# Kernel optimization log

Hardware: AMD Instinct MI355X
Metric: run time of the kernel (lower is better)

The kernel has to match this reference:

```python
import jax, jax.numpy as jnp
import numpy as np

NC, ND, B, K = 10000, 1000000, 8192, 64
EMB = 16
CH_DENSE, DEV_DENSE = 16, 20
CAT_MAX = [100, 4, 50, 200, 500, 1000, 300]  # lang, plat, os, country, carrier, brand, plat_os
H1, H2, ATTN_H = 64, 64, 84
IN1 = CH_DENSE + EMB        # 32  (channel dense + channel_id emb)
IN2 = DEV_DENSE + 7 * EMB   # 132 (device dense + 7 cat embs)


def setup_inputs() -> dict:
    key = jax.random.key(0)
    ks = jax.random.split(key, 32)
    def nrm(k, shape, s=0.05):
        return jax.random.normal(k, shape, dtype=jnp.float32) * s
    inp = {}
    inp["channel_dense"] = nrm(ks[0], (NC, CH_DENSE), 1.0)
    inp["device_dense"] = nrm(ks[1], (ND, DEV_DENSE), 1.0)
    inp["channel_id_emb"] = nrm(ks[2], (NC, EMB))
    names = ["lang_emb", "plat_emb", "os_emb", "country_emb", "carrier_emb", "brand_emb", "plat_os_emb"]
    for i, (n, m) in enumerate(zip(names, CAT_MAX)):
        inp[n] = nrm(ks[3 + i], (m, EMB))
    inp["W_agg"] = nrm(ks[10], (IN2, H2));  inp["b_agg"] = jnp.zeros((H2,), jnp.float32)
    inp["W_self"] = nrm(ks[11], (IN1, H1)); inp["b_self"] = jnp.zeros((H1,), jnp.float32)
    inp["W_attn"] = nrm(ks[12], (H2 + IN1, ATTN_H)); inp["b_attn"] = jnp.zeros((ATTN_H,), jnp.float32)
    inp["W_attn2"] = nrm(ks[13], (ATTN_H, 1)); inp["b_attn2"] = jnp.zeros((1,), jnp.float32)
    inp["channel_ids"] = jax.random.randint(ks[14], (NC,), 0, NC)
    cat_cols = [jax.random.randint(ks[15 + i], (ND,), 0, m) for i, m in enumerate(CAT_MAX)]
    inp["device_cat"] = jnp.stack(cat_cols, axis=1)  # [ND, 7]
    inp["vertices"] = jax.random.randint(ks[22], (B,), 0, NC)
    inp["bot_neibrs"] = jax.random.randint(ks[23], (B, K), 0, ND)
    inp["normal_neibrs"] = jax.random.randint(ks[24], (B, K), 0, ND)
    inp["bot_counts"] = jax.random.randint(ks[25], (B,), 1, K + 1)
    inp["normal_counts"] = jax.random.randint(ks[26], (B,), 1, K + 1)
    return inp


def reference(channel_dense, device_dense, channel_id_emb, lang_emb, plat_emb, os_emb,
              country_emb, carrier_emb, brand_emb, plat_os_emb,
              W_agg, b_agg, W_self, b_self, W_attn, b_attn, W_attn2, b_attn2,
              channel_ids, device_cat, vertices, bot_neibrs, normal_neibrs,
              bot_counts, normal_counts):
    cat_tables = [lang_emb, plat_emb, os_emb, country_emb, carrier_emb, brand_emb, plat_os_emb]
    # channel self features: dense cols + channel_id embedding  -> [B, IN1]
    ch_v = jnp.concatenate([channel_dense[vertices],
                            channel_id_emb[channel_ids[vertices]]], axis=1)

    def agg(neibrs, counts):
        # gather neighbor device features, embed categoricals, masked mean, linear (Mean_agg)
        dense = device_dense[neibrs]                                   # [B, K, DEV_DENSE]
        cats = device_cat[neibrs]                                      # [B, K, 7]
        embs = jnp.concatenate([t[cats[..., i]] for i, t in enumerate(cat_tables)], axis=-1)
        feats = jnp.concatenate([dense, embs], axis=-1)                # [B, K, IN2]
        mask = (jnp.arange(K)[None, :] < counts[:, None]).astype(feats.dtype)
        mean = jnp.sum(feats * mask[..., None], axis=1) / jnp.maximum(counts, 1).astype(feats.dtype)[:, None]
        return mean @ W_agg + b_agg                                    # [B, H2]

    bots = agg(bot_neibrs, bot_counts)
    normal = agg(normal_neibrs, normal_counts)

    def score(h):
        # attention MLP on concat(aggregated feats, channel self feats)
        return jax.nn.relu(jnp.concatenate([h, ch_v], axis=1) @ W_attn + b_attn) @ W_attn2 + b_attn2

    a = jax.nn.softmax(jnp.concatenate([score(bots), score(normal)], axis=1), axis=1)  # [B, 2]
    gcn = a[:, 0:1] * bots + a[:, 1:2] * normal                        # convex combination [B, H2]
    # Msg_out: relu(concat(agg_out, linear(self)))
    return jax.nn.relu(jnp.concatenate([gcn, ch_v @ W_self + b_self], axis=1))  # [B, H2+H1]
```

## Files before the change

### kernel.cpp

```cpp
#include <hip/hip_runtime.h>

#define BATCH 8192
#define KNB   64
#define EMB   16
#define CHD   16
#define DVD   20
#define H1    64
#define H2    64
#define AH    84
#define IN1   32
#define IN2   132

#define RB 32
#define VB 16

__global__ __launch_bounds__(256) void gconv_gather(
    const float* __restrict__ device_dense,
    const float* __restrict__ t0, const float* __restrict__ t1,
    const float* __restrict__ t2, const float* __restrict__ t3,
    const float* __restrict__ t4, const float* __restrict__ t5,
    const float* __restrict__ t6,
    const int* __restrict__ device_cat,
    const int* __restrict__ bot_neibrs,
    const int* __restrict__ normal_neibrs,
    const int* __restrict__ bot_counts,
    const int* __restrict__ normal_counts,
    float* __restrict__ fsum_ws)
{
    const int b    = blockIdx.x;
    const int v    = b >> 1;
    const int half = b & 1;
    const int t    = threadIdx.x;
    const int w    = t >> 6;
    const int L    = t & 63;

    __shared__ alignas(16) int   ofs[KNB][8];
    __shared__ alignas(16) float psum[4][IN2];

    const int* neibrs = half ? normal_neibrs : bot_neibrs;
    int cnt = half ? normal_counts[v] : bot_counts[v];
    if (cnt > KNB) cnt = KNB;
    if (cnt < 1)   cnt = 1;

    if (t < KNB) {
        int n = 0;
        if (t < cnt) n = neibrs[v * KNB + t];
        const long cb = (long)n * 7;
        const int c0 = device_cat[cb + 0];
        const int c1 = device_cat[cb + 1];
        const int c2 = device_cat[cb + 2];
        const int c3 = device_cat[cb + 3];
        const int c4 = device_cat[cb + 4];
        const int c5 = device_cat[cb + 5];
        const int c6 = device_cat[cb + 6];
        *(int4*)&ofs[t][0] = make_int4(n * DVD, c0 * EMB, c1 * EMB, c2 * EMB);
        *(int4*)&ofs[t][4] = make_int4(c3 * EMB, c4 * EMB, c5 * EMB, c6 * EMB);
    }
    __syncthreads();

    const int kk   = L >> 5;
    const int slot = L & 31;
    const float* P; int sIdx, c4v;
    if (slot < 5) {
        P = device_dense; sIdx = 0; c4v = slot * 4;
    } else {
        const int e = slot - 5;
        const int tsel = e >> 2;
        c4v = (e & 3) * 4; sIdx = 1 + tsel;
        switch (tsel) {
            case 0: P = t0; break;
            case 1: P = t1; break;
            case 2: P = t2; break;
            case 3: P = t3; break;
            case 4: P = t4; break;
            case 5: P = t5; break;
            default: P = t6; break;
        }
    }
    const bool xa = (slot == 0);

    float4 acc  = make_float4(0.f, 0.f, 0.f, 0.f);
    float4 accx = make_float4(0.f, 0.f, 0.f, 0.f);

    for (int i0 = 0; i0 < 8; i0 += 4) {
        if (2 * w + 8 * i0 >= cnt) break;
        int o[4], ox[4];
        #pragma unroll
        for (int i = 0; i < 4; ++i) {
            const int k = 2 * w + 8 * (i0 + i) + kk;
            o[i]  = ofs[k][sIdx];
            ox[i] = ofs[k][7];
        }
        __builtin_amdgcn_sched_barrier(0);
        float4 val[4], vx[4];
        #pragma unroll
        for (int i = 0; i < 4; ++i)
            val[i] = *(const float4*)(P + o[i] + c4v);
        if (xa) {
            #pragma unroll
            for (int i = 0; i < 4; ++i)
                vx[i] = *(const float4*)(t6 + ox[i] + 12);
        }
        __builtin_amdgcn_sched_barrier(0);
        #pragma unroll
        for (int i = 0; i < 4; ++i) {
            const int k = 2 * w + 8 * (i0 + i) + kk;
            const float m = (k < cnt) ? 1.f : 0.f;
            acc.x = fmaf(m, val[i].x, acc.x);
            acc.y = fmaf(m, val[i].y, acc.y);
            acc.z = fmaf(m, val[i].z, acc.z);
            acc.w = fmaf(m, val[i].w, acc.w);
            if (xa) {
                accx.x = fmaf(m, vx[i].x, accx.x);
                accx.y = fmaf(m, vx[i].y, accx.y);
                accx.z = fmaf(m, vx[i].z, accx.z);
                accx.w = fmaf(m, vx[i].w, accx.w);
            }
        }
    }

    acc.x += __shfl_xor(acc.x, 32, 64);
    acc.y += __shfl_xor(acc.y, 32, 64);
    acc.z += __shfl_xor(acc.z, 32, 64);
    acc.w += __shfl_xor(acc.w, 32, 64);
    accx.x += __shfl_xor(accx.x, 32, 64);
    accx.y += __shfl_xor(accx.y, 32, 64);
    accx.z += __shfl_xor(accx.z, 32, 64);
    accx.w += __shfl_xor(accx.w, 32, 64);

    if (L < 32) *(float4*)&psum[w][slot * 4] = acc;
    if (L == 0) *(float4*)&psum[w][128]      = accx;
    __syncthreads();

    if (t < IN2)
        fsum_ws[(size_t)b * IN2 + t] =
            psum[0][t] + psum[1][t] + psum[2][t] + psum[3][t];
}

__global__ __launch_bounds__(256) void gconv_dense(
    const float* __restrict__ channel_dense,
    const float* __restrict__ channel_id_emb,
    const float* __restrict__ W_agg,  const float* __restrict__ b_agg,
    const float* __restrict__ W_self, const float* __restrict__ b_self,
    const float* __restrict__ W_attn, const float* __restrict__ b_attn,
    const float* __restrict__ W_attn2,
    const int* __restrict__ channel_ids,
    const int* __restrict__ vertices,
    const int* __restrict__ bot_counts,
    const int* __restrict__ normal_counts,
    const float* __restrict__ fsum_ws,
    float* __restrict__ out)
{
    const int blk = blockIdx.x;
    const int b0  = blk * RB;
    const int v0  = blk * VB;
    const int t   = threadIdx.x;

    __shared__ alignas(16) float fs[RB][IN2];
    __shared__ alignas(16) float chvs[VB][IN1];
    __shared__ alignas(16) float hs[RB][H2];
    __shared__ float u_lds[AH][RB + 1];
    __shared__ float sarr[RB];
    __shared__ float cinv[RB];

    for (int idx = t; idx < RB * IN2 / 4; idx += 256) {
        const float4 vv = *(const float4*)(fsum_ws + (size_t)b0 * IN2 + idx * 4);
        *(float4*)&((float*)fs)[idx * 4] = vv;
    }
    if (t < RB) {
        const int b = b0 + t;
        const int v = b >> 1;
        int c = (b & 1) ? normal_counts[v] : bot_counts[v];
        c = (c > KNB) ? KNB : ((c < 1) ? 1 : c);
        cinv[t] = 1.0f / (float)c;
    }
    if (t < 128) {
        const int vx = t >> 3, q = t & 7;
        const int vert = vertices[v0 + vx];
        const float* src = (q < 4)
            ? channel_dense  + (size_t)vert * CHD + q * 4
            : channel_id_emb + (size_t)channel_ids[vert] * EMB + (q - 4) * 4;
        *(float4*)&chvs[vx][q * 4] = *(const float4*)src;
    }
    __syncthreads();

    {
        const int w = t >> 6, lane = t & 63;
        const int r0 = w * 8;
        float acc[8] = {0.f, 0.f, 0.f, 0.f, 0.f, 0.f, 0.f, 0.f};
        #pragma unroll 4
        for (int f = 0; f < IN2; ++f) {
            const float wv = W_agg[f * H2 + lane];
            #pragma unroll
            for (int r = 0; r < 8; ++r)
                acc[r] = fmaf(fs[r0 + r][f], wv, acc[r]);
        }
        const float bb = b_agg[lane];
        #pragma unroll
        for (int r = 0; r < 8; ++r)
            hs[r0 + r][lane] = fmaf(acc[r], cinv[r0 + r], bb);
    }
    __syncthreads();

    if (t < 2 * AH) {
        const int rg = (t >= AH) ? 1 : 0;
        const int aa = t - AH * rg;
        const int r0 = rg * 16;
        float acc[16];
        #pragma unroll
        for (int r = 0; r < 16; ++r) acc[r] = 0.f;
        #pragma unroll 2
        for (int f = 0; f < H2; ++f) {
            const float wv = W_attn[f * AH + aa];
            #pragma unroll
            for (int r = 0; r < 16; ++r)
                acc[r] = fmaf(hs[r0 + r][f], wv, acc[r]);
        }
        #pragma unroll 2
        for (int f = 0; f < IN1; ++f) {
            const float wv = W_attn[(H2 + f) * AH + aa];
            #pragma unroll
            for (int r = 0; r < 16; ++r)
                acc[r] = fmaf(chvs[(r0 + r) >> 1][f], wv, acc[r]);
        }
        const float ba = b_attn[aa], w2 = W_attn2[aa];
        #pragma unroll
        for (int r = 0; r < 16; ++r)
            u_lds[aa][r0 + r] = fmaxf(acc[r] + ba, 0.f) * w2;
    }
    __syncthreads();

    if (t < RB) {
        float s = 0.f;
        #pragma unroll 4
        for (int aa = 0; aa < AH; ++aa) s += u_lds[aa][t];
        sarr[t] = s;
    }
    __syncthreads();

    {
        const int vl = t >> 4;
        const int c8 = (t & 15) * 8;
        const float s0 = sarr[2 * vl], s1 = sarr[2 * vl + 1];
        const float mm = fmaxf(s0, s1);
        const float e0 = __expf(s0 - mm), e1 = __expf(s1 - mm);
        const float rs = 1.0f / (e0 + e1);
        const float a0 = e0 * rs, a1 = e1 * rs;
        float o[8];
        if (c8 < H2) {
            #pragma unroll
            for (int c = 0; c < 8; ++c)
                o[c] = fmaxf(a0 * hs[2 * vl][c8 + c] + a1 * hs[2 * vl + 1][c8 + c], 0.f);
        } else {
            const int cs = c8 - H2;
            float accS[8];
            #pragma unroll
            for (int c = 0; c < 8; ++c) accS[c] = b_self[cs + c];
            #pragma unroll 4
            for (int f = 0; f < IN1; ++f) {
                const float xv = chvs[vl][f];
                const float4 wa = *(const float4*)(W_self + f * H1 + cs);
                const float4 wb = *(const float4*)(W_self + f * H1 + cs + 4);
                accS[0] = fmaf(xv, wa.x, accS[0]);
                accS[1] = fmaf(xv, wa.y, accS[1]);
                accS[2] = fmaf(xv, wa.z, accS[2]);
                accS[3] = fmaf(xv, wa.w, accS[3]);
                accS[4] = fmaf(xv, wb.x, accS[4]);
                accS[5] = fmaf(xv, wb.y, accS[5]);
                accS[6] = fmaf(xv, wb.z, accS[6]);
                accS[7] = fmaf(xv, wb.w, accS[7]);
            }
            #pragma unroll
            for (int c = 0; c < 8; ++c) o[c] = fmaxf(accS[c], 0.f);
        }
        float4* op = (float4*)(out + (size_t)(v0 + vl) * (H1 + H2) + c8);
        op[0] = make_float4(o[0], o[1], o[2], o[3]);
        op[1] = make_float4(o[4], o[5], o[6], o[7]);
    }
}

extern "C" void kernel_launch(void* const* d_in, const int* in_sizes, int n_in,
                              void* d_out, int out_size, void* d_ws, size_t ws_size,
                              hipStream_t stream) {
    const float* channel_dense  = (const float*)d_in[0];
    const float* device_dense   = (const float*)d_in[1];
    const float* channel_id_emb = (const float*)d_in[2];
    const float* lang_emb       = (const float*)d_in[3];
    const float* plat_emb       = (const float*)d_in[4];
    const float* os_emb         = (const float*)d_in[5];
    const float* country_emb    = (const float*)d_in[6];
    const float* carrier_emb    = (const float*)d_in[7];
    const float* brand_emb      = (const float*)d_in[8];
    const float* plat_os_emb    = (const float*)d_in[9];
    const float* W_agg          = (const float*)d_in[10];
    const float* b_agg          = (const float*)d_in[11];
    const float* W_self         = (const float*)d_in[12];
    const float* b_self         = (const float*)d_in[13];
    const float* W_attn         = (const float*)d_in[14];
    const float* b_attn         = (const float*)d_in[15];
    const float* W_attn2        = (const float*)d_in[16];
    const int* channel_ids   = (const int*)d_in[18];
    const int* device_cat    = (const int*)d_in[19];
    const int* vertices      = (const int*)d_in[20];
    const int* bot_neibrs    = (const int*)d_in[21];
    const int* normal_neibrs = (const int*)d_in[22];
    const int* bot_counts    = (const int*)d_in[23];
    const int* normal_counts = (const int*)d_in[24];

    float* fsum_ws = (float*)d_ws;
    float* out     = (float*)d_out;

    gconv_gather<<<dim3(2 * BATCH), dim3(256), 0, stream>>>(
        device_dense, lang_emb, plat_emb, os_emb, country_emb, carrier_emb,
        brand_emb, plat_os_emb, device_cat, bot_neibrs, normal_neibrs,
        bot_counts, normal_counts, fsum_ws);

    gconv_dense<<<dim3(2 * BATCH / RB), dim3(256), 0, stream>>>(
        channel_dense, channel_id_emb, W_agg, b_agg, W_self, b_self,
        W_attn, b_attn, W_attn2, channel_ids, vertices,
        bot_counts, normal_counts, fsum_ws, out);
}
```

Before: 76.81 us.

## Process multiple rows per gather block with double-buffered index staging and LDS plat table

Each gather block now handles eight (vertex, half) rows instead of one. It prefetches the next row's neighbor and category offsets into a second shared buffer while accumulating the current row. The tiny 4-row platform embedding table is cached in LDS, and its lookups are served by otherwise-idle lanes, which removes the extra lane-0 global load. Category indices are loaded as two overlapping int4 vectors. This cuts launch and block-setup overhead and hides index-fetch latency, at the cost of extra barriers per row and fewer total blocks for latency hiding.

```diff
diff --git a/kernel.cpp b/kernel.cpp
--- a/kernel.cpp
+++ b/kernel.cpp
@@ -13,6 +13,8 @@
 
 #define RB 32
 #define VB 16
+#define NIT 8
+#define NBLK (2 * BATCH / NIT)
 
 __global__ __launch_bounds__(256) void gconv_gather(
     const float* __restrict__ device_dense,
@@ -27,114 +29,144 @@
     const int* __restrict__ normal_counts,
     float* __restrict__ fsum_ws)
 {
-    const int b    = blockIdx.x;
-    const int v    = b >> 1;
-    const int half = b & 1;
+    const int blk  = blockIdx.x;
     const int t    = threadIdx.x;
     const int w    = t >> 6;
     const int L    = t & 63;
-
-    __shared__ alignas(16) int   ofs[KNB][8];
-    __shared__ alignas(16) float psum[4][IN2];
-
-    const int* neibrs = half ? normal_neibrs : bot_neibrs;
-    int cnt = half ? normal_counts[v] : bot_counts[v];
-    if (cnt > KNB) cnt = KNB;
-    if (cnt < 1)   cnt = 1;
-
-    if (t < KNB) {
-        int n = 0;
-        if (t < cnt) n = neibrs[v * KNB + t];
-        const long cb = (long)n * 7;
-        const int c0 = device_cat[cb + 0];
-        const int c1 = device_cat[cb + 1];
-        const int c2 = device_cat[cb + 2];
-        const int c3 = device_cat[cb + 3];
-        const int c4 = device_cat[cb + 4];
-        const int c5 = device_cat[cb + 5];
-        const int c6 = device_cat[cb + 6];
-        *(int4*)&ofs[t][0] = make_int4(n * DVD, c0 * EMB, c1 * EMB, c2 * EMB);
-        *(int4*)&ofs[t][4] = make_int4(c3 * EMB, c4 * EMB, c5 * EMB, c6 * EMB);
-    }
-    __syncthreads();
-
     const int kk   = L >> 5;
     const int slot = L & 31;
-    const float* P; int sIdx, c4v;
-    if (slot < 5) {
-        P = device_dense; sIdx = 0; c4v = slot * 4;
-    } else {
-        const int e = slot - 5;
-        const int tsel = e >> 2;
-        c4v = (e & 3) * 4; sIdx = 1 + tsel;
-        switch (tsel) {
+
+    __shared__ alignas(16) int   ofs[2][KNB][8];
+    __shared__ alignas(16) float psum[4][IN2];
+    __shared__ alignas(16) float plat_lds[64];
+    __shared__ int scnt[2];
+
+    if (t < 64) plat_lds[t] = t1[t];
+
+    const float* P = device_dense;
+    int sIdx = 0, c4v = slot * 4, fb = slot * 4;
+    if (slot >= 5 && slot < 29) {
+        const int e  = slot - 5;
+        const int tb = e >> 2;
+        c4v  = (e & 3) * 4;
+        sIdx = (tb == 0) ? 1 : (tb + 2);
+        fb   = 20 + 16 * ((tb == 0) ? 0 : tb + 1) + c4v;
+        switch (tb) {
             case 0: P = t0; break;
-            case 1: P = t1; break;
-            case 2: P = t2; break;
-            case 3: P = t3; break;
-            case 4: P = t4; break;
-            case 5: P = t5; break;
+            case 1: P = t2; break;
+            case 2: P = t3; break;
+            case 3: P = t4; break;
+            case 4: P = t5; break;
             default: P = t6; break;
         }
     }
-    const bool xa = (slot == 0);
-
-    float4 acc  = make_float4(0.f, 0.f, 0.f, 0.f);
-    float4 accx = make_float4(0.f, 0.f, 0.f, 0.f);
-
-    for (int i0 = 0; i0 < 8; i0 += 4) {
-        if (2 * w + 8 * i0 >= cnt) break;
-        int o[4], ox[4];
+    const bool isPlat = (slot >= 29);
+    const int  pcol   = (slot - 29) * 4;
+    if (isPlat) fb = 36 + pcol;
+
+    auto stage = [&](int it, int buf) {
+        if (w != (it & 3)) return;
+        const int b  = blk * NIT + it;
+        const int v  = b >> 1;
+        const bool nh = b & 1;
+        int cnt = nh ? normal_counts[v] : bot_counts[v];
+        cnt = cnt < 1 ? 1 : (cnt > KNB ? KNB : cnt);
+        int n = 0;
+        if (L < cnt) n = (nh ? normal_neibrs : bot_neibrs)[v * KNB + L];
+        const long cb = (long)n * 7;
+        const int4 cA = *(const int4*)(device_cat + cb);
+        const int4 cB = *(const int4*)(device_cat + cb + 3);
+        *(int4*)&ofs[buf][L][0] = make_int4(n * DVD, cA.x * EMB, cA.y * EMB, cA.z * EMB);
+        *(int4*)&ofs[buf][L][4] = make_int4(cA.w * EMB, cB.y * EMB, cB.z * EMB, cB.w * EMB);
+        if (L == 0) scnt[buf] = cnt;
+    };
+
+    stage(0, 0);
+    __syncthreads();
+
+    int buf = 0;
+    for (int it = 0; it < NIT; ++it) {
+        if (it + 1 < NIT) stage(it + 1, buf ^ 1);
+
+        const int cnt = scnt[buf];
+        float4 acc  = make_float4(0.f, 0.f, 0.f, 0.f);
+        float4 accx = make_float4(0.f, 0.f, 0.f, 0.f);
+
         #pragma unroll
-        for (int i = 0; i < 4; ++i) {
-            const int k = 2 * w + 8 * (i0 + i) + kk;
-            o[i]  = ofs[k][sIdx];
-            ox[i] = ofs[k][7];
-        }
-        __builtin_amdgcn_sched_barrier(0);
-        float4 val[4], vx[4];
-        #pragma unroll
-        for (int i = 0; i < 4; ++i)
-            val[i] = *(const float4*)(P + o[i] + c4v);
-        if (xa) {
-            #pragma unroll
-            for (int i = 0; i < 4; ++i)
-                vx[i] = *(const float4*)(t6 + ox[i] + 12);
-        }
-        __builtin_amdgcn_sched_barrier(0);
-        #pragma unroll
-        for (int i = 0; i < 4; ++i) {
-            const int k = 2 * w + 8 * (i0 + i) + kk;
-            const float m = (k < cnt) ? 1.f : 0.f;
-            acc.x = fmaf(m, val[i].x, acc.x);
-            acc.y = fmaf(m, val[i].y, acc.y);
-            acc.z = fmaf(m, val[i].z, acc.z);
-            acc.w = fmaf(m, val[i].w, acc.w);
-            if (xa) {
-                accx.x = fmaf(m, vx[i].x, accx.x);
-                accx.y = fmaf(m, vx[i].y, accx.y);
-                accx.z = fmaf(m, vx[i].z, accx.z);
-                accx.w = fmaf(m, vx[i].w, accx.w);
+        for (int c0 = 0; c0 < 8; c0 += 4) {
+            if (2 * w + 8 * c0 >= cnt) break;
+            const int kb = 2 * w + kk;
+            if (!isPlat) {
+                int o[4];
+                #pragma unroll
+                for (int i = 0; i < 4; ++i)
+                    o[i] = ofs[buf][kb + 8 * (c0 + i)][sIdx];
+                __builtin_amdgcn_sched_barrier(0);
+                float4 val[4];
+                #pragma unroll
+                for (int i = 0; i < 4; ++i)
+                    val[i] = *(const float4*)(P + o[i] + c4v);
+                __builtin_amdgcn_sched_barrier(0);
+                #pragma unroll
+                for (int i = 0; i < 4; ++i) {
+                    const float m = (kb + 8 * (c0 + i) < cnt) ? 1.f : 0.f;
+                    acc.x = fmaf(m, val[i].x, acc.x);
+                    acc.y = fmaf(m, val[i].y, acc.y);
+                    acc.z = fmaf(m, val[i].z, acc.z);
+                    acc.w = fmaf(m, val[i].w, acc.w);
+                }
+            } else {
+                #pragma unroll
+                for (int i = 0; i < 4; ++i) {
+                    const int k = kb + 8 * (c0 + i);
+                    const int o = ofs[buf][k][2];
+                    const float m = (k < cnt) ? 1.f : 0.f;
+                    const float4 pv = *(const float4*)&plat_lds[o + pcol];
+                    acc.x = fmaf(m, pv.x, acc.x);
+                    acc.y = fmaf(m, pv.y, acc.y);
+                    acc.z = fmaf(m, pv.z, acc.z);
+                    acc.w = fmaf(m, pv.w, acc.w);
+                    if (slot == 29) {
+                        const float4 pw = *(const float4*)&plat_lds[o + 12];
+                        accx.x = fmaf(m, pw.x, accx.x);
+                        accx.y = fmaf(m, pw.y, accx.y);
+                        accx.z = fmaf(m, pw.z, accx.z);
+                        accx.w = fmaf(m, pw.w, accx.w);
+                    }
+                }
             }
         }
-    }
-
-    acc.x += __shfl_xor(acc.x, 32, 64);
-    acc.y += __shfl_xor(acc.y, 32, 64);
-    acc.z += __shfl_xor(acc.z, 32, 64);
-    acc.w += __shfl_xor(acc.w, 32, 64);
-    accx.x += __shfl_xor(accx.x, 32, 64);
-    accx.y += __shfl_xor(accx.y, 32, 64);
-    accx.z += __shfl_xor(accx.z, 32, 64);
-    accx.w += __shfl_xor(accx.w, 32, 64);
-
-    if (L < 32) *(float4*)&psum[w][slot * 4] = acc;
-    if (L == 0) *(float4*)&psum[w][128]      = accx;
-    __syncthreads();
-
-    if (t < IN2)
-        fsum_ws[(size_t)b * IN2 + t] =
-            psum[0][t] + psum[1][t] + psum[2][t] + psum[3][t];
+
+        acc.x += __shfl_xor(acc.x, 32, 64);
+        acc.y += __shfl_xor(acc.y, 32, 64);
+        acc.z += __shfl_xor(acc.z, 32, 64);
+        acc.w += __shfl_xor(acc.w, 32, 64);
+        accx.x += __shfl_xor(accx.x, 32, 64);
+        accx.y += __shfl_xor(accx.y, 32, 64);
+        accx.z += __shfl_xor(accx.z, 32, 64);
+        accx.w += __shfl_xor(accx.w, 32, 64);
+
+        if (L < 32) {
+            *(float4*)&psum[w][fb] = acc;
+            if (slot == 29) *(float4*)&psum[w][48] = accx;
+        }
+        __syncthreads();
+
+        if (t < IN2 / 4) {
+            const float4 p0 = *(const float4*)&psum[0][t * 4];
+            const float4 p1 = *(const float4*)&psum[1][t * 4];
+            const float4 p2 = *(const float4*)&psum[2][t * 4];
+            const float4 p3 = *(const float4*)&psum[3][t * 4];
+            const int b = blk * NIT + it;
+            *(float4*)(fsum_ws + (size_t)b * IN2 + t * 4) =
+                make_float4(p0.x + p1.x + p2.x + p3.x,
+                            p0.y + p1.y + p2.y + p3.y,
+                            p0.z + p1.z + p2.z + p3.z,
+                            p0.w + p1.w + p2.w + p3.w);
+        }
+        __syncthreads();
+        buf ^= 1;
+    }
 }
 
 __global__ __launch_bounds__(256) void gconv_dense(
@@ -310,7 +342,7 @@
     float* fsum_ws = (float*)d_ws;
     float* out     = (float*)d_out;
 
-    gconv_gather<<<dim3(2 * BATCH), dim3(256), 0, stream>>>(
+    gconv_gather<<<dim3(NBLK), dim3(256), 0, stream>>>(
         device_dense, lang_emb, plat_emb, os_emb, country_emb, carrier_emb,
         brand_emb, plat_os_emb, device_cat, bot_neibrs, normal_neibrs,
         bot_counts, normal_counts, fsum_ws);
```

Measured after the change: 75.98 us. About the same (-1.1%).

## Assign one wavefront per neighbor list in gather kernel, removing block syncs

Applied to the files above, without the earlier changes.

The gather kernel now gives each wavefront its own (vertex, half) item, so one block of four wavefronts handles four items instead of one. Each wave builds its own offset table in LDS and waits on lgkmcnt instead of a block barrier. It loops over all its neighbors with an 8-deep unrolled load batch and writes results straight to the workspace, with no cross-wave LDS reduction. The leftover 16-byte slot of the last table is now computed with a full wave shuffle reduction, and the category reads are vectorized int4 loads. The intent is to remove __syncthreads and block-level reduction overhead and to raise memory-level parallelism per wave. The cost is that each wave now does more serial work per item. The int4 load at offset cb+3 reads misaligned addresses, and LDS writes and reads are not fenced across lanes except through the waitcnt.

```diff
diff --git a/kernel.cpp b/kernel.cpp
--- a/kernel.cpp
+++ b/kernel.cpp
@@ -27,47 +27,42 @@
     const int* __restrict__ normal_counts,
     float* __restrict__ fsum_ws)
 {
-    const int b    = blockIdx.x;
-    const int v    = b >> 1;
-    const int half = b & 1;
     const int t    = threadIdx.x;
     const int w    = t >> 6;
     const int L    = t & 63;
-
-    __shared__ alignas(16) int   ofs[KNB][8];
-    __shared__ alignas(16) float psum[4][IN2];
-
-    const int* neibrs = half ? normal_neibrs : bot_neibrs;
-    int cnt = half ? normal_counts[v] : bot_counts[v];
-    if (cnt > KNB) cnt = KNB;
-    if (cnt < 1)   cnt = 1;
-
-    if (t < KNB) {
-        int n = 0;
-        if (t < cnt) n = neibrs[v * KNB + t];
-        const long cb = (long)n * 7;
-        const int c0 = device_cat[cb + 0];
-        const int c1 = device_cat[cb + 1];
-        const int c2 = device_cat[cb + 2];
-        const int c3 = device_cat[cb + 3];
-        const int c4 = device_cat[cb + 4];
-        const int c5 = device_cat[cb + 5];
-        const int c6 = device_cat[cb + 6];
-        *(int4*)&ofs[t][0] = make_int4(n * DVD, c0 * EMB, c1 * EMB, c2 * EMB);
-        *(int4*)&ofs[t][4] = make_int4(c3 * EMB, c4 * EMB, c5 * EMB, c6 * EMB);
-    }
-    __syncthreads();
-
     const int kk   = L >> 5;
     const int slot = L & 31;
-    const float* P; int sIdx, c4v;
+    const int item = blockIdx.x * 4 + w;
+    const int v    = item >> 1;
+
+    __shared__ alignas(16) int ofs[4][KNB][8];
+
+    int cnt = (item & 1) ? normal_counts[v] : bot_counts[v];
+    cnt = cnt < 1 ? 1 : (cnt > KNB ? KNB : cnt);
+    cnt = __builtin_amdgcn_readfirstlane(cnt);
+
+    {
+        const int* nb = (item & 1) ? normal_neibrs : bot_neibrs;
+        const int n = (L < cnt) ? nb[v * KNB + L] : 0;
+        const long cb = (long)n * 7;
+        const int4 cA = *(const int4*)(device_cat + cb);
+        const int4 cB = *(const int4*)(device_cat + cb + 3);
+        *(int4*)&ofs[w][L][0] = make_int4(n * DVD, cA.x * EMB, cA.y * EMB, cA.z * EMB);
+        *(int4*)&ofs[w][L][4] = make_int4(cA.w * EMB, cB.y * EMB, cB.z * EMB, cB.w * EMB);
+    }
+    __asm__ volatile("s_waitcnt lgkmcnt(0)" ::: "memory");
+    __builtin_amdgcn_sched_barrier(0);
+
+    const float* P;
+    int oIdx, col, feat;
     if (slot < 5) {
-        P = device_dense; sIdx = 0; c4v = slot * 4;
+        P = device_dense; oIdx = 0; col = slot * 4; feat = slot * 4;
     } else {
-        const int e = slot - 5;
-        const int tsel = e >> 2;
-        c4v = (e & 3) * 4; sIdx = 1 + tsel;
-        switch (tsel) {
+        const int e  = slot - 5;
+        const int tb = e >> 2;
+        const int q  = e & 3;
+        oIdx = 1 + tb; col = 4 * q; feat = 20 + 16 * tb + 4 * q;
+        switch (tb) {
             case 0: P = t0; break;
             case 1: P = t1; break;
             case 2: P = t2; break;
@@ -77,45 +72,27 @@
             default: P = t6; break;
         }
     }
-    const bool xa = (slot == 0);
-
-    float4 acc  = make_float4(0.f, 0.f, 0.f, 0.f);
-    float4 accx = make_float4(0.f, 0.f, 0.f, 0.f);
-
-    for (int i0 = 0; i0 < 8; i0 += 4) {
-        if (2 * w + 8 * i0 >= cnt) break;
-        int o[4], ox[4];
-        #pragma unroll
-        for (int i = 0; i < 4; ++i) {
-            const int k = 2 * w + 8 * (i0 + i) + kk;
-            o[i]  = ofs[k][sIdx];
-            ox[i] = ofs[k][7];
-        }
+
+    float4 acc = make_float4(0.f, 0.f, 0.f, 0.f);
+    const int passes = (cnt + 1) >> 1;
+    for (int pc = 0; pc < passes; pc += 8) {
+        int o[8];
+        #pragma unroll
+        for (int j = 0; j < 8; ++j)
+            o[j] = ofs[w][2 * (pc + j) + kk][oIdx];
         __builtin_amdgcn_sched_barrier(0);
-        float4 val[4], vx[4];
-        #pragma unroll
-        for (int i = 0; i < 4; ++i)
-            val[i] = *(const float4*)(P + o[i] + c4v);
-        if (xa) {
-            #pragma unroll
-            for (int i = 0; i < 4; ++i)
-                vx[i] = *(const float4*)(t6 + ox[i] + 12);
-        }
+        float4 val[8];
+        #pragma unroll
+        for (int j = 0; j < 8; ++j)
+            val[j] = *(const float4*)(P + o[j] + col);
         __builtin_amdgcn_sched_barrier(0);
         #pragma unroll
-        for (int i = 0; i < 4; ++i) {
-            const int k = 2 * w + 8 * (i0 + i) + kk;
-            const float m = (k < cnt) ? 1.f : 0.f;
-            acc.x = fmaf(m, val[i].x, acc.x);
-            acc.y = fmaf(m, val[i].y, acc.y);
-            acc.z = fmaf(m, val[i].z, acc.z);
-            acc.w = fmaf(m, val[i].w, acc.w);
-            if (xa) {
-                accx.x = fmaf(m, vx[i].x, accx.x);
-                accx.y = fmaf(m, vx[i].y, accx.y);
-                accx.z = fmaf(m, vx[i].z, accx.z);
-                accx.w = fmaf(m, vx[i].w, accx.w);
-            }
+        for (int j = 0; j < 8; ++j) {
+            const float m = (2 * (pc + j) + kk < cnt) ? 1.f : 0.f;
+            acc.x = fmaf(m, val[j].x, acc.x);
+            acc.y = fmaf(m, val[j].y, acc.y);
+            acc.z = fmaf(m, val[j].z, acc.z);
+            acc.w = fmaf(m, val[j].w, acc.w);
         }
     }
 
@@ -123,18 +100,25 @@
     acc.y += __shfl_xor(acc.y, 32, 64);
     acc.z += __shfl_xor(acc.z, 32, 64);
     acc.w += __shfl_xor(acc.w, 32, 64);
-    accx.x += __shfl_xor(accx.x, 32, 64);
-    accx.y += __shfl_xor(accx.y, 32, 64);
-    accx.z += __shfl_xor(accx.z, 32, 64);
-    accx.w += __shfl_xor(accx.w, 32, 64);
-
-    if (L < 32) *(float4*)&psum[w][slot * 4] = acc;
-    if (L == 0) *(float4*)&psum[w][128]      = accx;
-    __syncthreads();
-
-    if (t < IN2)
-        fsum_ws[(size_t)b * IN2 + t] =
-            psum[0][t] + psum[1][t] + psum[2][t] + psum[3][t];
+
+    {
+        const int o32 = ofs[w][L][7];
+        const float4 vx = *(const float4*)(t6 + o32 + 12);
+        const float m = (L < cnt) ? 1.f : 0.f;
+        float4 ax = make_float4(m * vx.x, m * vx.y, m * vx.z, m * vx.w);
+        #pragma unroll
+        for (int off = 1; off < 64; off <<= 1) {
+            ax.x += __shfl_xor(ax.x, off, 64);
+            ax.y += __shfl_xor(ax.y, off, 64);
+            ax.z += __shfl_xor(ax.z, off, 64);
+            ax.w += __shfl_xor(ax.w, off, 64);
+        }
+        if (L == 0)
+            *(float4*)(fsum_ws + (size_t)item * IN2 + 128) = ax;
+    }
+
+    if (L < 32)
+        *(float4*)(fsum_ws + (size_t)item * IN2 + feat) = acc;
 }
 
 __global__ __launch_bounds__(256) void gconv_dense(
@@ -310,7 +294,7 @@
     float* fsum_ws = (float*)d_ws;
     float* out     = (float*)d_out;
 
-    gconv_gather<<<dim3(2 * BATCH), dim3(256), 0, stream>>>(
+    gconv_gather<<<dim3(2 * BATCH / 4), dim3(256), 0, stream>>>(
         device_dense, lang_emb, plat_emb, os_emb, country_emb, carrier_emb,
         brand_emb, plat_os_emb, device_cat, bot_neibrs, normal_neibrs,
         bot_counts, normal_counts, fsum_ws);
```

New measurement: 72.09 us. 1.07x faster.
